# Kernel tuning notes

Measured on AMD Instinct MI355X. Metric: run time of the kernel, lower is better.

## Reference

```python
import jax, jax.numpy as jnp
import numpy as np

EPS = 1e-15
MAXN = 1.0 - 1e-5  # projection radius for c=1 Poincare ball

def _norm(x):
    return jnp.sqrt(jnp.clip(jnp.sum(x * x, axis=-1, keepdims=True), EPS))

def _artanh(x):
    return jnp.arctanh(jnp.clip(x, -1.0 + 1e-7, 1.0 - 1e-7))

def projx(x):
    n = _norm(x)
    return jnp.where(n > MAXN, x * (MAXN / n), x)

def expmap0(v):
    n = _norm(v)
    return jnp.tanh(n) * v / n

def logmap0(x):
    n = _norm(x)
    return _artanh(n) * x / n

def mobius_add(x, y):
    x2 = jnp.sum(x * x, -1, keepdims=True)
    y2 = jnp.sum(y * y, -1, keepdims=True)
    xy = jnp.sum(x * y, -1, keepdims=True)
    num = (1.0 + 2.0 * xy + y2) * x + (1.0 - x2) * y
    den = 1.0 + 2.0 * xy + x2 * y2
    return num / jnp.clip(den, EPS)

def _lam(x):
    return 2.0 / jnp.clip(1.0 - jnp.sum(x * x, -1, keepdims=True), EPS)

def expmap(x, v):
    n = _norm(v)
    second = jnp.tanh(_lam(x) * n / 2.0) * v / n
    return projx(mobius_add(x, second))

def logmap(x, y):
    u = mobius_add(-x, y)
    n = _norm(u)
    return (2.0 / _lam(x)) * _artanh(n) * u / n

def mobius_matvec(W, x):
    mx = x @ W.T
    xn = _norm(x)
    mxn = _norm(mx)
    return jnp.tanh(mxn / xn * _artanh(xn)) * mx / mxn

def setup_inputs() -> dict:
    key = jax.random.key(0)
    ks = jax.random.split(key, 8)
    B, L, F = 128, 336, 128
    SEG, D, H, T = 24, 128, 256, 8
    return {
        "x": jax.random.normal(ks[0], (B, L, F), jnp.float32),
        "revin_w": jnp.ones((F,), jnp.float32),
        "revin_b": jnp.zeros((F,), jnp.float32),
        "W_enc": jax.random.normal(ks[1], (SEG, D), jnp.float32) * 0.05,
        "b_enc": jax.random.normal(ks[2], (D,), jnp.float32) * 0.01,
        "W_vel": jax.random.normal(ks[3], (D, D), jnp.float32) * (1.0 / np.sqrt(D)),
        "b_vel": jax.random.normal(ks[4], (D,), jnp.float32) * 0.01,
        "step_sizes": jnp.array(1.0, jnp.float32),
        "W1": jax.random.normal(ks[5], (D, H), jnp.float32) * (1.0 / np.sqrt(D)),
        "b1": jnp.zeros((H,), jnp.float32),
        "W2": jax.random.normal(ks[6], (H, SEG), jnp.float32) * (1.0 / np.sqrt(H)),
        "b2": jnp.zeros((SEG,), jnp.float32),
    }

def reference(x, revin_w, revin_b, W_enc, b_enc, W_vel, b_vel, step_sizes, W1, b1, W2, b2):
    B, L, F = x.shape
    SEG = W_enc.shape[0]
    D = W_enc.shape[1]
    N = L // SEG            # 14 history segments
    T = 192 // SEG          # 8 prediction segments
    # RevIN norm (per-series stats over time)
    mu = jnp.mean(x, axis=1, keepdims=True)            # [B,1,F]
    std = jnp.sqrt(jnp.var(x, axis=1, keepdims=True) + 1e-5)
    xn = (x - mu) / std * revin_w + revin_b
    # channel-independent: [B*F, N, SEG]
    xb = xn.transpose(0, 2, 1).reshape(B * F, N, SEG)
    # segment encoder -> Poincare ball
    z = projx(expmap0(xb @ W_enc + b_enc))             # [BF,N,D]
    # initial velocity from discounted logmap differences
    vels = logmap(z[:, :-1, :], z[:, 1:, :])           # [BF,N-1,D]
    w = 0.9 ** (N - 2 - jnp.arange(N - 1, dtype=x.dtype))
    w = w / jnp.sum(w)
    v_init = jnp.mean(vels * w[None, :, None], axis=1)  # [BF,D]
    z0 = z[:, -1, :]
    # PoincareLinear velocity net: mobius matvec + bias point + projection
    v0t = projx(mobius_add(mobius_matvec(W_vel, v_init), expmap0(b_vel)))
    step = jax.nn.sigmoid(step_sizes)
    t_vals = jnp.arange(1, T + 1, dtype=x.dtype)
    v_all = step * t_vals[None, :, None] * v0t[:, None, :]  # [BF,T,D]
    z_fut = expmap(z0[:, None, :], v_all)                   # [BF,T,D]
    # shared reconstruction head in tangent space at origin
    tan = logmap0(z_fut)
    h = jax.nn.relu(tan @ W1 + b1)
    out = h @ W2 + b2                                       # [BF,T,SEG]
    pred = out.reshape(B, F, T * SEG).transpose(0, 2, 1)    # [B,pred_len,F]
    # RevIN denorm
    pred = (pred - revin_b) / revin_w * std + mu
    return pred
```

## Files before the change

### kernel.cpp

```cpp
#include <hip/hip_runtime.h>
#include <hip/hip_bf16.h>

#define EPSF 1e-15f
#define MAXNF 0.99999f

typedef __attribute__((ext_vector_type(8))) short short8v;
typedef __attribute__((ext_vector_type(8))) ushort ushort8v;
typedef __attribute__((ext_vector_type(4))) float f32x4;

__device__ __forceinline__ float wave_sum(float v) {
#pragma unroll
    for (int off = 32; off > 0; off >>= 1) v += __shfl_xor(v, off, 64);
    return v;
}
__device__ __forceinline__ float rcpf(float x) { return __builtin_amdgcn_rcpf(x); }
__device__ __forceinline__ float tanh_g(float x) {
    if (x < 0.03f) return x * (1.f - 0.33333333f * x * x);
    float e = __expf(-2.f * x);
    return (1.f - e) * rcpf(1.f + e);
}
__device__ __forceinline__ float atanh_g(float x) {
    if (x < 0.03f) return x * (1.f + 0.33333333f * x * x);
    return 0.5f * __logf((1.f + x) * rcpf(1.f - x));
}
__device__ __forceinline__ float tanh_b(float x) {
    float e = __expf(-2.f * x);
    float tv = (1.f - e) * rcpf(1.f + e);
    float sv = x * (1.f - 0.33333333f * x * x);
    return (x < 0.03f) ? sv : tv;
}
__device__ __forceinline__ float atanh_b(float x) {
    float lv = 0.5f * __logf((1.f + x) * rcpf(1.f - x));
    float sv = x * (1.f + 0.33333333f * x * x);
    return (x < 0.03f) ? sv : lv;
}
__device__ __forceinline__ ushort f2bf(float f) {
    uint32_t u = __float_as_uint(f);
    uint32_t r = (u + 0x7fffu + ((u >> 16) & 1u)) >> 16;
    return (ushort)r;
}
__device__ __forceinline__ float bf2f(ushort u) { return __uint_as_float(((uint32_t)u) << 16); }

__global__ __launch_bounds__(256) void k_prep(
    const float* __restrict__ W1, const float* __restrict__ W2,
    const float* __restrict__ W_vel, const float* __restrict__ b_vel,
    const float* __restrict__ W_enc, const float* __restrict__ b_enc,
    ushort* __restrict__ W1t, ushort* __restrict__ W2tp,
    ushort* __restrict__ WB25h, ushort* __restrict__ WB25l,
    ushort* __restrict__ MB25h, ushort* __restrict__ MB25l,
    float* __restrict__ gq,
    float* __restrict__ cvec, float* __restrict__ scp) {
    int bid = blockIdx.x, tid = threadIdx.x;
    if (bid == 0) {
        __shared__ float red[4];
        float v = (tid < 128) ? b_vel[tid] : 0.f;
        float p = wave_sum(v * v);
        if ((tid & 63) == 0) red[tid >> 6] = p;
        __syncthreads();
        float ssq = red[0] + red[1] + red[2] + red[3];
        float nn = sqrtf(fmaxf(ssq, EPSF));
        float th = tanhf(nn);
        if (tid < 128) cvec[tid] = th / nn * v;
        if (tid == 0) scp[0] = th * th;
    } else if (bid <= 128) {
        int idx = (bid - 1) * 256 + tid;
        int n = idx >> 7, k = idx & 127;
        W1t[idx] = f2bf(W1[k * 256 + n]);
    } else if (bid <= 160) {
        int idx = (bid - 129) * 256 + tid;
        int s = idx >> 8, j = idx & 255;
        W2tp[idx] = (s < 24) ? f2bf(W2[j * 24 + s]) : (ushort)0;
    } else if (bid <= 176) {
        int idx = (bid - 161) * 256 + tid;
        int d = idx >> 5, s = idx & 31;
        float val = (s < 24) ? W_enc[s * 128 + d] : (s == 24 ? b_enc[d] : 0.f);
        ushort h = f2bf(val);
        WB25h[idx] = h;
        WB25l[idx] = f2bf(val - bf2f(h));
    } else if (bid <= 327) {
        int o = (bid - 177) * 4 + (tid >> 6);
        int lane = tid & 63;
        if (o < 601) {
            const float* pa; const float* pb;
            if (o < 576)      { pa = W_enc + (o / 24) * 128; pb = W_enc + (o % 24) * 128; }
            else if (o < 600) { pa = W_enc + (o - 576) * 128; pb = b_enc; }
            else              { pa = b_enc; pb = b_enc; }
            float2 a = *(const float2*)(pa + lane * 2);
            float2 c = *(const float2*)(pb + lane * 2);
            float p = wave_sum(a.x * c.x + a.y * c.y);
            if (lane == 0) gq[o] = p;
        }
    } else {
        int j = (bid - 328) * 4 + (tid >> 6);
        int lane = tid & 63;
        float2 wv = *(const float2*)(W_vel + j * 128 + lane * 2);
        for (int s = 0; s < 25; ++s) {
            const float* pa = (s < 24) ? (W_enc + s * 128) : b_enc;
            float2 a = *(const float2*)(pa + lane * 2);
            float p = wave_sum(wv.x * a.x + wv.y * a.y);
            if (lane == 0) {
                ushort h = f2bf(p);
                MB25h[j * 32 + s] = h;
                MB25l[j * 32 + s] = f2bf(p - bf2f(h));
            }
        }
        if (lane >= 25 && lane < 32) { MB25h[j * 32 + lane] = 0; MB25l[j * 32 + lane] = 0; }
    }
}

__global__ __launch_bounds__(256) void k_gvf(
    const float* __restrict__ x,
    const float* __restrict__ revin_w, const float* __restrict__ revin_b,
    const float* __restrict__ gq, ushort* __restrict__ Avz,
    const ushort* __restrict__ WB25h, const ushort* __restrict__ WB25l,
    const ushort* __restrict__ MB25h, const ushort* __restrict__ MB25l,
    const float* __restrict__ cvec, const float* __restrict__ scp,
    const float* __restrict__ step_sizes, ushort* __restrict__ tanb,
    float* __restrict__ osc_o, float* __restrict__ osh_o) {
    __shared__ __align__(16) char smem[50688];
    float* xall = (float*)smem;
    float* psm  = (float*)(smem + 44352);
    float* ps2m = (float*)(smem + 45376);
    float* scs  = (float*)(smem + 46400);
    float* shs  = (float*)(smem + 46528);
    float* zs   = (float*)smem;
    float* vsb  = (float*)(smem + 16896);
    float* msb  = (float*)(smem + 33792);

    int bidx = blockIdx.x;
    int b = bidx >> 2, f0 = (bidx & 3) * 32;
    int tid = threadIdx.x;
    int fi = tid & 31, g = tid >> 5;
    {
        float s = 0.f, s2 = 0.f;
        for (int k = 0; k < 42; ++k) {
            int l = g + 8 * k;
            float v = x[((size_t)b * 336 + l) * 128 + f0 + fi];
            xall[l * 33 + fi] = v;
            s += v; s2 += v * v;
        }
        psm[g * 32 + fi] = s; ps2m[g * 32 + fi] = s2;
    }
    __syncthreads();
    if (tid < 32) {
        float S = 0.f, S2 = 0.f;
#pragma unroll
        for (int h = 0; h < 8; ++h) { S += psm[h * 32 + tid]; S2 += ps2m[h * 32 + tid]; }
        float m = S * (1.f / 336.f);
        float var = S2 * (1.f / 336.f) - m * m;
        float sd = sqrtf(var + 1e-5f);
        int ff = f0 + tid;
        float rw = revin_w[ff], rb = revin_b[ff];
        float sc = rw * rcpf(sd);
        scs[tid] = sc;
        shs[tid] = rb - m * sc;
        float ocv = sd * rcpf(rw);
        osc_o[b * 128 + ff] = ocv;
        osh_o[b * 128 + ff] = m - rb * ocv;
    }
    __syncthreads();
    {
        float sc = scs[fi], sh = shs[fi];
        for (int k = 0; k < 42; ++k) {
            int l = g + 8 * k;
            xall[l * 33 + fi] = xall[l * 33 + fi] * sc + sh;
        }
    }
    int lane = tid & 63, w = tid >> 6;
    int f = w * 8 + (lane >> 3), p = lane & 7;
    int t0 = 3 * p;
    float Greg[3][24], wbr[3];
#pragma unroll
    for (int i = 0; i < 3; ++i) {
#pragma unroll
        for (int s3 = 0; s3 < 24; ++s3) Greg[i][s3] = gq[(t0 + i) * 24 + s3];
        wbr[i] = gq[576 + t0 + i];
    }
    float bb = gq[600];
    __syncthreads();

    float pd1a[14], pwa[14], pd2a[14];
    {
        float xp0 = 0.f, xp1 = 0.f, xp2 = 0.f;
#pragma unroll
        for (int n = 0; n < 14; ++n) {
            float g0 = 0.f, g1 = 0.f, g2 = 0.f;
#pragma unroll
            for (int s3 = 0; s3 < 24; ++s3) {
                float xv = xall[(n * 24 + s3) * 33 + f];
                g0 += Greg[0][s3] * xv; g1 += Greg[1][s3] * xv; g2 += Greg[2][s3] * xv;
            }
            float xm0 = xall[(n * 24 + t0) * 33 + f];
            float xm1 = xall[(n * 24 + t0 + 1) * 33 + f];
            float xm2 = xall[(n * 24 + t0 + 2) * 33 + f];
            float pd1 = g0 * xm0 + g1 * xm1 + g2 * xm2;
            float pw  = wbr[0] * xm0 + wbr[1] * xm1 + wbr[2] * xm2;
            float pd2 = g0 * xp0 + g1 * xp1 + g2 * xp2;
#pragma unroll
            for (int off = 1; off < 8; off <<= 1) {
                pd1 += __shfl_xor(pd1, off, 64);
                pd2 += __shfl_xor(pd2, off, 64);
                pw  += __shfl_xor(pw, off, 64);
            }
            pd1a[n] = pd1; pwa[n] = pw; pd2a[n] = pd2;
            xp0 = xm0; xp1 = xm1; xp2 = xm2;
        }
    }
    float wsum = 0.f; { float pp = 1.f; for (int k2 = 0; k2 < 13; ++k2) { wsum += pp; pp *= 0.9f; } }
    float wi; { float pp = 1.f; for (int k2 = 0; k2 < 12; ++k2) pp *= 0.9f; wi = pp / (wsum * 13.f); }
    float c[14];
#pragma unroll
    for (int m = 0; m < 14; ++m) c[m] = 0.f;
    float sczp = 0.f, szp = 0.f, pwprev = 0.f;
#pragma unroll
    for (int n = 0; n < 14; ++n) {
        float pd1 = pd1a[n], pw = pwa[n], pd2 = pd2a[n];
        float ssq = pd1 + 2.f * pw + bb;
        float nn = sqrtf(fmaxf(ssq, EPSF));
        float th = tanh_g(nn);
        float scz, sz;
        if (th > MAXNF) { scz = MAXNF * rcpf(nn); sz = MAXNF * MAXNF; }
        else            { scz = th * rcpf(nn);    sz = th * th; }
        if (n > 0) {
            float dotup = pd2 + pwprev + pw + bb;
            float xyp = sczp * scz * dotup;
            float t2 = 1.f - 2.f * xyp;
            float den = fmaxf(t2 + szp * sz, EPSF);
            float rden = rcpf(den);
            float a1 = t2 + sz, a2 = 1.f - szp;
            float usq = (a1 * a1 * szp - 2.f * a1 * a2 * xyp + a2 * a2 * sz) * (rden * rden);
            float un = sqrtf(fmaxf(usq, EPSF));
            float art = atanh_g(fminf(un, 1.f - 1e-7f));
            float fac = fmaxf(a2, EPSF) * art * rcpf(un) * rden * wi;
            c[n - 1] += -fac * a1 * sczp;
            c[n]     +=  fac * a2 * scz;
            wi *= (1.f / 0.9f);
        }
        sczp = scz; szp = sz; pwprev = pw;
    }
    float s_v = 0.f;
#pragma unroll
    for (int m = 0; m < 14; ++m) s_v += c[m];
    float sczL = sczp;
    size_t rbase = ((size_t)(b * 128 + f0 + f)) * 128;
#pragma unroll
    for (int q = 0; q < 4; ++q) {
        int u = 4 * p + q;
        float vv, vz;
        if (u < 24) {
            float acc = 0.f;
#pragma unroll
            for (int n = 0; n < 14; ++n) acc += c[n] * xall[(n * 24 + u) * 33 + f];
            vv = acc;
            vz = sczL * xall[(312 + u) * 33 + f];
        } else if (u == 24) { vv = s_v; vz = sczL; }
        else { vv = 0.f; vz = 0.f; }
        ushort vh = f2bf(vv); ushort vl = f2bf(vv - bf2f(vh));
        ushort zh = f2bf(vz); ushort zl = f2bf(vz - bf2f(zh));
        Avz[rbase + u] = vh;
        Avz[rbase + 32 + u] = vl;
        Avz[rbase + 64 + u] = zh;
        Avz[rbase + 96 + u] = zl;
    }
    __syncthreads();

    int lrow = lane & 15, lk = lane >> 4;
    int r0 = bidx * 32;
    short8v BWh[2], BWl[2], BMh[2], BMl[2];
#pragma unroll
    for (int dt = 0; dt < 2; ++dt) {
        int d = w * 32 + dt * 16 + lrow;
        BWh[dt] = *(const short8v*)(WB25h + d * 32 + lk * 8);
        BWl[dt] = *(const short8v*)(WB25l + d * 32 + lk * 8);
        BMh[dt] = *(const short8v*)(MB25h + d * 32 + lk * 8);
        BMl[dt] = *(const short8v*)(MB25l + d * 32 + lk * 8);
    }
#pragma unroll
    for (int rg = 0; rg < 2; ++rg) {
        const ushort* ap = Avz + (size_t)(r0 + rg * 16 + lrow) * 128;
        short8v Avh = *(const short8v*)(ap + lk * 8);
        short8v Avl = *(const short8v*)(ap + 32 + lk * 8);
        short8v Azh = *(const short8v*)(ap + 64 + lk * 8);
        short8v Azl = *(const short8v*)(ap + 96 + lk * 8);
#pragma unroll
        for (int dt = 0; dt < 2; ++dt) {
            f32x4 aV = (f32x4)(0.f), aZ = (f32x4)(0.f), aM = (f32x4)(0.f);
            aV = __builtin_amdgcn_mfma_f32_16x16x32_bf16(Avh, BWh[dt], aV, 0, 0, 0);
            aV = __builtin_amdgcn_mfma_f32_16x16x32_bf16(Avh, BWl[dt], aV, 0, 0, 0);
            aV = __builtin_amdgcn_mfma_f32_16x16x32_bf16(Avl, BWh[dt], aV, 0, 0, 0);
            aZ = __builtin_amdgcn_mfma_f32_16x16x32_bf16(Azh, BWh[dt], aZ, 0, 0, 0);
            aZ = __builtin_amdgcn_mfma_f32_16x16x32_bf16(Azh, BWl[dt], aZ, 0, 0, 0);
            aZ = __builtin_amdgcn_mfma_f32_16x16x32_bf16(Azl, BWh[dt], aZ, 0, 0, 0);
            aM = __builtin_amdgcn_mfma_f32_16x16x32_bf16(Avh, BMh[dt], aM, 0, 0, 0);
            aM = __builtin_amdgcn_mfma_f32_16x16x32_bf16(Avh, BMl[dt], aM, 0, 0, 0);
            aM = __builtin_amdgcn_mfma_f32_16x16x32_bf16(Avl, BMh[dt], aM, 0, 0, 0);
            int d = w * 32 + dt * 16 + lrow;
#pragma unroll
            for (int j = 0; j < 4; ++j) {
                int row = rg * 16 + lk * 4 + j;
                vsb[row * 132 + d] = aV[j];
                zs[row * 132 + d] = aZ[j];
                msb[row * 132 + d] = aM[j];
            }
        }
    }
    __syncthreads();
    float scc = scp[0];
    float step = rcpf(1.f + __expf(-step_sizes[0]));
    float2 cv = *(const float2*)&cvec[lane * 2];
    float tl = (float)((lane & 7) + 1);
    uint* t32 = (uint*)tanb;
    for (int q = 0; q < 8; ++q) {
        int rl = w * 8 + q;
        int r = r0 + rl;
        float2 vi = *(const float2*)&vsb[rl * 132 + lane * 2];
        float2 mx = *(const float2*)&msb[rl * 132 + lane * 2];
        float2 z0 = *(const float2*)&zs[rl * 132 + lane * 2];
        float xn2  = wave_sum(vi.x * vi.x + vi.y * vi.y);
        float mxn2 = wave_sum(mx.x * mx.x + mx.y * mx.y);
        float mxc  = wave_sum(mx.x * cv.x + mx.y * cv.y);
        float z0mx = wave_sum(z0.x * mx.x + z0.y * mx.y);
        float z0c  = wave_sum(z0.x * cv.x + z0.y * cv.y);
        float x2   = wave_sum(z0.x * z0.x + z0.y * z0.y);
        float xn = sqrtf(fmaxf(xn2, EPSF));
        float mxn = sqrtf(fmaxf(mxn2, EPSF));
        float artx = atanh_g(fminf(xn, 1.f - 1e-7f));
        float tm = tanh_g(mxn * rcpf(xn) * artx);
        float scm = tm * rcpf(mxn);
        float sm = tm * tm;
        float xy2 = scm * mxc;
        float den2 = fmaxf(1.f + 2.f * xy2 + sm * scc, EPSF);
        float rd2 = rcpf(den2);
        float A2 = (1.f + 2.f * xy2 + scc) * scm * rd2;
        float B2 = (1.f - sm) * rd2;
        float v0n2 = A2 * A2 * mxn2 + 2.f * A2 * B2 * mxc + B2 * B2 * scc;
        float nv0 = sqrtf(fmaxf(v0n2, EPSF));
        if (nv0 > MAXNF) { float pf = MAXNF * rcpf(nv0); A2 *= pf; B2 *= pf; nv0 = MAXNF; }
        v0n2 = nv0 * nv0;
        float inv_nv0 = rcpf(nv0);
        float zdv = A2 * z0mx + B2 * z0c;
        float v00 = A2 * mx.x + B2 * cv.x, v01 = A2 * mx.y + B2 * cv.y;
        float il = rcpf(fmaxf(1.f - x2, EPSF));
        float nt_ = step * tl * nv0;
        float th = tanh_b(nt_ * il);
        float xy = th * inv_nv0 * zdv;
        float y2 = th * th;
        float den = fmaxf(1.f + 2.f * xy + x2 * y2, EPSF);
        float rd = rcpf(den);
        float A = (1.f + 2.f * xy + y2) * rd;
        float B = (1.f - x2) * th * inv_nv0 * rd;
        float rsq = A * A * x2 + 2.f * A * B * zdv + B * B * v0n2;
        float nr = sqrtf(fmaxf(rsq, EPSF));
        float pf2 = (nr > MAXNF) ? MAXNF * rcpf(nr) : 1.f;
        A *= pf2; B *= pf2; nr = fminf(nr, MAXNF);
        float art = atanh_b(fminf(nr, 1.f - 1e-7f));
        float tf = art * rcpf(nr);
        float FA = tf * A, FB = tf * B;
        int bbv = r >> 7, ff = r & 127;
#pragma unroll
        for (int t = 0; t < 8; ++t) {
            float FAt = __shfl(FA, t);
            float FBt = __shfl(FB, t);
            uint pk = (uint)f2bf(FAt * z0.x + FBt * v00) | ((uint)f2bf(FAt * z0.y + FBt * v01) << 16);
            t32[((size_t)(bbv * 1024 + t * 128 + ff)) * 64 + lane] = pk;
        }
    }
}

__global__ __launch_bounds__(256, 2) void k_head(
    const ushort* __restrict__ tanb, const ushort* __restrict__ W1t, const float* __restrict__ b1,
    const ushort* __restrict__ W2tp, const float* __restrict__ b2,
    const float* __restrict__ osc_i, const float* __restrict__ osh_i,
    float* __restrict__ out) {
    __shared__ __align__(16) ushort hs[64][264];
    int tid = threadIdx.x;
    int wid = tid >> 6, lane = tid & 63;
    int lrow = lane & 15, lk = lane >> 4;

    short8v Bw[4][4];
#pragma unroll
    for (int nt = 0; nt < 4; ++nt) {
        const ushort* wp = W1t + (size_t)((wid * 4 + nt) * 16 + lrow) * 128 + lk * 8;
#pragma unroll
        for (int kk = 0; kk < 4; ++kk) Bw[nt][kk] = *(const short8v*)(wp + kk * 32);
    }
    float b1v[4];
#pragma unroll
    for (int nt = 0; nt < 4; ++nt) b1v[nt] = b1[(wid * 4 + nt) * 16 + lrow];
    float b2a = (lrow < 24) ? b2[lrow] : 0.f;
    float b2bv = (lrow < 8) ? b2[16 + lrow] : 0.f;

    int tile0 = blockIdx.x * 4;
    int bbk = tile0 >> 4;
    int fr = wid * 16 + lk * 4;
    f32x4 oc0 = *(const f32x4*)&osc_i[bbk * 128 + fr];
    f32x4 oh0 = *(const f32x4*)&osh_i[bbk * 128 + fr];
    f32x4 oc1 = *(const f32x4*)&osc_i[bbk * 128 + 64 + fr];
    f32x4 oh1 = *(const f32x4*)&osh_i[bbk * 128 + 64 + fr];

    short8v A[4][4];
    {
        const ushort* tp = tanb + ((size_t)tile0 * 64 + lrow) * 128 + lk * 8;
#pragma unroll
        for (int rg = 0; rg < 4; ++rg)
#pragma unroll
            for (int kk = 0; kk < 4; ++kk)
                A[rg][kk] = *(const short8v*)(tp + (size_t)rg * 2048 + kk * 32);
    }
#pragma unroll
    for (int it = 0; it < 4; ++it) {
        int tile = tile0 + it;
        f32x4 acc[4][4];
#pragma unroll
        for (int rg = 0; rg < 4; ++rg)
#pragma unroll
            for (int nt = 0; nt < 4; ++nt) acc[rg][nt] = (f32x4)(0.f);
#pragma unroll
        for (int kk = 0; kk < 4; ++kk)
#pragma unroll
            for (int rg = 0; rg < 4; ++rg)
#pragma unroll
                for (int nt = 0; nt < 4; ++nt)
                    acc[rg][nt] = __builtin_amdgcn_mfma_f32_16x16x32_bf16(A[rg][kk], Bw[nt][kk], acc[rg][nt], 0, 0, 0);
        __syncthreads();
#pragma unroll
        for (int rg = 0; rg < 4; ++rg)
#pragma unroll
            for (int nt = 0; nt < 4; ++nt)
#pragma unroll
                for (int j = 0; j < 4; ++j)
                    hs[rg * 16 + lk * 4 + j][(wid * 4 + nt) * 16 + lrow] =
                        f2bf(fmaxf(acc[rg][nt][j] + b1v[nt], 0.f));
        __syncthreads();
        if (it + 1 < 4) {
            const ushort* tp = tanb + ((size_t)(tile + 1) * 64 + lrow) * 128 + lk * 8;
#pragma unroll
            for (int rg = 0; rg < 4; ++rg)
#pragma unroll
                for (int kk = 0; kk < 4; ++kk)
                    A[rg][kk] = *(const short8v*)(tp + (size_t)rg * 2048 + kk * 32);
        }
        f32x4 acc2[2];
        acc2[0] = (f32x4)(0.f); acc2[1] = (f32x4)(0.f);
#pragma unroll
        for (int kk2 = 0; kk2 < 8; ++kk2) {
            short8v Ah = *(const short8v*)&hs[wid * 16 + lrow][kk2 * 32 + lk * 8];
#pragma unroll
            for (int nt2 = 0; nt2 < 2; ++nt2) {
                short8v Bv = *(const short8v*)(W2tp + (size_t)(nt2 * 16 + lrow) * 256 + kk2 * 32 + lk * 8);
                acc2[nt2] = __builtin_amdgcn_mfma_f32_16x16x32_bf16(Ah, Bv, acc2[nt2], 0, 0, 0);
            }
        }
        int rem = tile & 15, tt = rem >> 1, fhalf = rem & 1;
        f32x4 oc = fhalf ? oc1 : oc0;
        f32x4 oh = fhalf ? oh1 : oh0;
        int f0 = fhalf << 6;
#pragma unroll
        for (int nt2 = 0; nt2 < 2; ++nt2) {
            int col = nt2 * 16 + lrow;
            if (col < 24) {
                float bb2 = (nt2 == 0) ? b2a : b2bv;
                f32x4 v = acc2[nt2];
                v[0] = (v[0] + bb2) * oc[0] + oh[0];
                v[1] = (v[1] + bb2) * oc[1] + oh[1];
                v[2] = (v[2] + bb2) * oc[2] + oh[2];
                v[3] = (v[3] + bb2) * oc[3] + oh[3];
                *(f32x4*)&out[((size_t)bbk * 192 + tt * 24 + col) * 128 + f0 + fr] = v;
            }
        }
    }
}

extern "C" void kernel_launch(void* const* d_in, const int* in_sizes, int n_in,
                              void* d_out, int out_size, void* d_ws, size_t ws_size,
                              hipStream_t stream) {
    (void)in_sizes; (void)n_in; (void)out_size; (void)ws_size;
    const float* x          = (const float*)d_in[0];
    const float* revin_w    = (const float*)d_in[1];
    const float* revin_b    = (const float*)d_in[2];
    const float* W_enc      = (const float*)d_in[3];
    const float* b_enc      = (const float*)d_in[4];
    const float* W_vel      = (const float*)d_in[5];
    const float* b_vel      = (const float*)d_in[6];
    const float* step_sizes = (const float*)d_in[7];
    const float* W1         = (const float*)d_in[8];
    const float* b1         = (const float*)d_in[9];
    const float* W2         = (const float*)d_in[10];
    const float* b2         = (const float*)d_in[11];
    float* out = (float*)d_out;

    float* wsf   = (float*)d_ws;
    float* osc   = wsf;
    float* osh   = osc + 16384;
    float* cvec  = osh + 16384;
    float* scp   = cvec + 128;
    float* gq    = scp + 64;
    ushort* W1t   = (ushort*)(gq + 640);
    ushort* W2tp  = W1t + 32768;
    ushort* WB25h = W2tp + 8192;
    ushort* WB25l = WB25h + 4096;
    ushort* MB25h = WB25l + 4096;
    ushort* MB25l = MB25h + 4096;
    ushort* Avz   = MB25l + 4096;
    ushort* tanb  = Avz + (size_t)16384 * 128;

    k_prep<<<dim3(360), dim3(256), 0, stream>>>(W1, W2, W_vel, b_vel, W_enc, b_enc,
                                                W1t, W2tp, WB25h, WB25l, MB25h, MB25l,
                                                gq, cvec, scp);
    k_gvf<<<dim3(512), dim3(256), 0, stream>>>(x, revin_w, revin_b, gq, Avz,
                                               WB25h, WB25l, MB25h, MB25l,
                                               cvec, scp, step_sizes, tanb, osc, osh);
    k_head<<<dim3(512), dim3(256), 0, stream>>>(tanb, W1t, b1, W2tp, b2, osc, osh, out);
}
```

Baseline: 90.19 us.

## Halve features per block in k_gvf to double grid and cut LDS

```diff
diff --git a/kernel.cpp b/kernel.cpp
--- a/kernel.cpp
+++ b/kernel.cpp
@@ -117,35 +117,35 @@
     const float* __restrict__ cvec, const float* __restrict__ scp,
     const float* __restrict__ step_sizes, ushort* __restrict__ tanb,
     float* __restrict__ osc_o, float* __restrict__ osh_o) {
-    __shared__ __align__(16) char smem[50688];
+    __shared__ __align__(16) char smem[25344];
     float* xall = (float*)smem;
-    float* psm  = (float*)(smem + 44352);
-    float* ps2m = (float*)(smem + 45376);
-    float* scs  = (float*)(smem + 46400);
-    float* shs  = (float*)(smem + 46528);
+    float* psm  = (float*)(smem + 22848);
+    float* ps2m = (float*)(smem + 23872);
+    float* scs  = (float*)(smem + 24896);
+    float* shs  = (float*)(smem + 24960);
     float* zs   = (float*)smem;
-    float* vsb  = (float*)(smem + 16896);
-    float* msb  = (float*)(smem + 33792);
+    float* vsb  = (float*)(smem + 8448);
+    float* msb  = (float*)(smem + 16896);
 
     int bidx = blockIdx.x;
-    int b = bidx >> 2, f0 = (bidx & 3) * 32;
+    int b = bidx >> 3, f0 = (bidx & 7) * 16;
     int tid = threadIdx.x;
-    int fi = tid & 31, g = tid >> 5;
+    int fi = tid & 15, g = tid >> 4;
     {
         float s = 0.f, s2 = 0.f;
-        for (int k = 0; k < 42; ++k) {
-            int l = g + 8 * k;
+        for (int k = 0; k < 21; ++k) {
+            int l = g + 16 * k;
             float v = x[((size_t)b * 336 + l) * 128 + f0 + fi];
-            xall[l * 33 + fi] = v;
+            xall[l * 17 + fi] = v;
             s += v; s2 += v * v;
         }
-        psm[g * 32 + fi] = s; ps2m[g * 32 + fi] = s2;
+        psm[g * 16 + fi] = s; ps2m[g * 16 + fi] = s2;
     }
     __syncthreads();
-    if (tid < 32) {
+    if (tid < 16) {
         float S = 0.f, S2 = 0.f;
 #pragma unroll
-        for (int h = 0; h < 8; ++h) { S += psm[h * 32 + tid]; S2 += ps2m[h * 32 + tid]; }
+        for (int h = 0; h < 16; ++h) { S += psm[h * 16 + tid]; S2 += ps2m[h * 16 + tid]; }
         float m = S * (1.f / 336.f);
         float var = S2 * (1.f / 336.f) - m * m;
         float sd = sqrtf(var + 1e-5f);
@@ -161,17 +161,19 @@
     __syncthreads();
     {
         float sc = scs[fi], sh = shs[fi];
-        for (int k = 0; k < 42; ++k) {
-            int l = g + 8 * k;
-            xall[l * 33 + fi] = xall[l * 33 + fi] * sc + sh;
+        for (int k = 0; k < 21; ++k) {
+            int l = g + 16 * k;
+            xall[l * 17 + fi] = xall[l * 17 + fi] * sc + sh;
         }
     }
     int lane = tid & 63, w = tid >> 6;
-    int f = w * 8 + (lane >> 3), p = lane & 7;
-    int t0 = 3 * p;
-    float Greg[3][24], wbr[3];
-#pragma unroll
-    for (int i = 0; i < 3; ++i) {
+    int floc = w * 4 + (lane >> 4), p = lane & 15;
+    int act = (p < 12) ? 1 : 0;
+    int t0 = act ? 2 * p : 0;
+    float mk = (float)act;
+    float Greg[2][24], wbr[2];
+#pragma unroll
+    for (int i = 0; i < 2; ++i) {
 #pragma unroll
         for (int s3 = 0; s3 < 24; ++s3) Greg[i][s3] = gq[(t0 + i) * 24 + s3];
         wbr[i] = gq[576 + t0 + i];
@@ -181,29 +183,28 @@
 
     float pd1a[14], pwa[14], pd2a[14];
     {
-        float xp0 = 0.f, xp1 = 0.f, xp2 = 0.f;
+        float xp0 = 0.f, xp1 = 0.f;
 #pragma unroll
         for (int n = 0; n < 14; ++n) {
-            float g0 = 0.f, g1 = 0.f, g2 = 0.f;
+            float g0 = 0.f, g1 = 0.f;
 #pragma unroll
             for (int s3 = 0; s3 < 24; ++s3) {
-                float xv = xall[(n * 24 + s3) * 33 + f];
-                g0 += Greg[0][s3] * xv; g1 += Greg[1][s3] * xv; g2 += Greg[2][s3] * xv;
+                float xv = xall[(n * 24 + s3) * 17 + floc];
+                g0 += Greg[0][s3] * xv; g1 += Greg[1][s3] * xv;
             }
-            float xm0 = xall[(n * 24 + t0) * 33 + f];
-            float xm1 = xall[(n * 24 + t0 + 1) * 33 + f];
-            float xm2 = xall[(n * 24 + t0 + 2) * 33 + f];
-            float pd1 = g0 * xm0 + g1 * xm1 + g2 * xm2;
-            float pw  = wbr[0] * xm0 + wbr[1] * xm1 + wbr[2] * xm2;
-            float pd2 = g0 * xp0 + g1 * xp1 + g2 * xp2;
-#pragma unroll
-            for (int off = 1; off < 8; off <<= 1) {
+            float xm0 = xall[(n * 24 + t0) * 17 + floc];
+            float xm1 = xall[(n * 24 + t0 + 1) * 17 + floc];
+            float pd1 = mk * (g0 * xm0 + g1 * xm1);
+            float pw  = mk * (wbr[0] * xm0 + wbr[1] * xm1);
+            float pd2 = mk * (g0 * xp0 + g1 * xp1);
+#pragma unroll
+            for (int off = 1; off < 16; off <<= 1) {
                 pd1 += __shfl_xor(pd1, off, 64);
                 pd2 += __shfl_xor(pd2, off, 64);
                 pw  += __shfl_xor(pw, off, 64);
             }
             pd1a[n] = pd1; pwa[n] = pw; pd2a[n] = pd2;
-            xp0 = xm0; xp1 = xm1; xp2 = xm2;
+            xp0 = xm0; xp1 = xm1;
         }
     }
     float wsum = 0.f; { float pp = 1.f; for (int k2 = 0; k2 < 13; ++k2) { wsum += pp; pp *= 0.9f; } }
@@ -242,17 +243,17 @@
 #pragma unroll
     for (int m = 0; m < 14; ++m) s_v += c[m];
     float sczL = sczp;
-    size_t rbase = ((size_t)(b * 128 + f0 + f)) * 128;
-#pragma unroll
-    for (int q = 0; q < 4; ++q) {
-        int u = 4 * p + q;
+    size_t rbase = ((size_t)(b * 128 + f0 + floc)) * 128;
+#pragma unroll
+    for (int q = 0; q < 2; ++q) {
+        int u = 2 * p + q;
         float vv, vz;
         if (u < 24) {
             float acc = 0.f;
 #pragma unroll
-            for (int n = 0; n < 14; ++n) acc += c[n] * xall[(n * 24 + u) * 33 + f];
+            for (int n = 0; n < 14; ++n) acc += c[n] * xall[(n * 24 + u) * 17 + floc];
             vv = acc;
-            vz = sczL * xall[(312 + u) * 33 + f];
+            vz = sczL * xall[(312 + u) * 17 + floc];
         } else if (u == 24) { vv = s_v; vz = sczL; }
         else { vv = 0.f; vz = 0.f; }
         ushort vh = f2bf(vv); ushort vl = f2bf(vv - bf2f(vh));
@@ -265,7 +266,7 @@
     __syncthreads();
 
     int lrow = lane & 15, lk = lane >> 4;
-    int r0 = bidx * 32;
+    int r0 = bidx * 16;
     short8v BWh[2], BWl[2], BMh[2], BMl[2];
 #pragma unroll
     for (int dt = 0; dt < 2; ++dt) {
@@ -275,9 +276,8 @@
         BMh[dt] = *(const short8v*)(MB25h + d * 32 + lk * 8);
         BMl[dt] = *(const short8v*)(MB25l + d * 32 + lk * 8);
     }
-#pragma unroll
-    for (int rg = 0; rg < 2; ++rg) {
-        const ushort* ap = Avz + (size_t)(r0 + rg * 16 + lrow) * 128;
+    {
+        const ushort* ap = Avz + (size_t)(r0 + lrow) * 128;
         short8v Avh = *(const short8v*)(ap + lk * 8);
         short8v Avl = *(const short8v*)(ap + 32 + lk * 8);
         short8v Azh = *(const short8v*)(ap + 64 + lk * 8);
@@ -297,7 +297,7 @@
             int d = w * 32 + dt * 16 + lrow;
 #pragma unroll
             for (int j = 0; j < 4; ++j) {
-                int row = rg * 16 + lk * 4 + j;
+                int row = lk * 4 + j;
                 vsb[row * 132 + d] = aV[j];
                 zs[row * 132 + d] = aZ[j];
                 msb[row * 132 + d] = aM[j];
@@ -310,8 +310,8 @@
     float2 cv = *(const float2*)&cvec[lane * 2];
     float tl = (float)((lane & 7) + 1);
     uint* t32 = (uint*)tanb;
-    for (int q = 0; q < 8; ++q) {
-        int rl = w * 8 + q;
+    for (int q = 0; q < 4; ++q) {
+        int rl = w * 4 + q;
         int r = r0 + rl;
         float2 vi = *(const float2*)&vsb[rl * 132 + lane * 2];
         float2 mx = *(const float2*)&msb[rl * 132 + lane * 2];
@@ -507,8 +507,8 @@
     k_prep<<<dim3(360), dim3(256), 0, stream>>>(W1, W2, W_vel, b_vel, W_enc, b_enc,
                                                 W1t, W2tp, WB25h, WB25l, MB25h, MB25l,
                                                 gq, cvec, scp);
-    k_gvf<<<dim3(512), dim3(256), 0, stream>>>(x, revin_w, revin_b, gq, Avz,
-                                               WB25h, WB25l, MB25h, MB25l,
-                                               cvec, scp, step_sizes, tanb, osc, osh);
+    k_gvf<<<dim3(1024), dim3(256), 0, stream>>>(x, revin_w, revin_b, gq, Avz,
+                                                WB25h, WB25l, MB25h, MB25l,
+                                                cvec, scp, step_sizes, tanb, osc, osh);
     k_head<<<dim3(512), dim3(256), 0, stream>>>(tanb, W1t, b1, W2tp, b2, osc, osh, out);
 }
```

Result: slower. 102.7 us (+13.8%).
